# Performance work log

Hardware: AMD Instinct MI355X
Metric: run time of the kernel (lower is better)

Reference implementation:

```python
import jax, jax.numpy as jnp
import numpy as np

N_NODES = 50000
N_EDGES = 400000
N_GRAPHS = 32
EMB = 64
EDGE_DIM = 4
IN_DIM = 11
LAYERS = 4
EPS = 1e-5


def _bn(x, g, b):
    # BatchNorm1d in train mode: biased batch statistics over rows
    m = jnp.mean(x, axis=0)
    v = jnp.mean(jnp.square(x - m), axis=0)
    return g * (x - m) * jax.lax.rsqrt(v + EPS) + b


def setup_inputs() -> dict:
    key = jax.random.key(0)
    ks = jax.random.split(key, 16)
    x = jax.random.normal(ks[0], (N_NODES, IN_DIM), dtype=jnp.float32)
    edge_attr = jax.random.normal(ks[1], (N_EDGES, EDGE_DIM), dtype=jnp.float32)
    edge_index = jax.random.randint(ks[2], (2, N_EDGES), 0, N_NODES, dtype=jnp.int32)
    batch = jnp.sort(jax.random.randint(ks[3], (N_NODES,), 0, N_GRAPHS, dtype=jnp.int32))

    def lin(k, fan_in, shape):
        bound = 1.0 / np.sqrt(fan_in)
        return jax.random.uniform(k, shape, jnp.float32, -bound, bound)

    msg_in = 2 * EMB + EDGE_DIM  # 132
    upd_in = 2 * EMB             # 128
    kk = jax.random.split(ks[4], 12)
    params = dict(
        lin_in_W=lin(kk[0], IN_DIM, (IN_DIM, EMB)),
        lin_in_b=lin(kk[1], IN_DIM, (EMB,)),
        msg_W1=lin(kk[2], msg_in, (LAYERS, msg_in, EMB)),
        msg_b1=lin(kk[3], msg_in, (LAYERS, EMB)),
        msg_g1=jnp.ones((LAYERS, EMB), jnp.float32),
        msg_be1=jnp.zeros((LAYERS, EMB), jnp.float32),
        msg_W2=lin(kk[4], EMB, (LAYERS, EMB, EMB)),
        msg_b2=lin(kk[5], EMB, (LAYERS, EMB)),
        msg_g2=jnp.ones((LAYERS, EMB), jnp.float32),
        msg_be2=jnp.zeros((LAYERS, EMB), jnp.float32),
        upd_W1=lin(kk[6], upd_in, (LAYERS, upd_in, EMB)),
        upd_b1=lin(kk[7], upd_in, (LAYERS, EMB)),
        upd_g1=jnp.ones((LAYERS, EMB), jnp.float32),
        upd_be1=jnp.zeros((LAYERS, EMB), jnp.float32),
        upd_W2=lin(kk[8], EMB, (LAYERS, EMB, EMB)),
        upd_b2=lin(kk[9], EMB, (LAYERS, EMB)),
        upd_g2=jnp.ones((LAYERS, EMB), jnp.float32),
        upd_be2=jnp.zeros((LAYERS, EMB), jnp.float32),
        pred_W=lin(kk[10], EMB, (EMB, 1)),
        pred_b=lin(kk[11], EMB, (1,)),
    )
    return dict(x=x, edge_attr=edge_attr, edge_index=edge_index, batch=batch, **params)


def reference(x, edge_attr, edge_index, batch, lin_in_W, lin_in_b,
              msg_W1, msg_b1, msg_g1, msg_be1, msg_W2, msg_b2, msg_g2, msg_be2,
              upd_W1, upd_b1, upd_g1, upd_be1, upd_W2, upd_b2, upd_g2, upd_be2,
              pred_W, pred_b):
    src = edge_index[0]  # j (source)
    dst = edge_index[1]  # i (target, PyG default flow source_to_target)
    h = x @ lin_in_W + lin_in_b  # (n, d)
    for l in range(LAYERS):
        m_in = jnp.concatenate([h[dst], h[src], edge_attr], axis=-1)  # (e, 2d+d_e)
        m = jax.nn.relu(_bn(m_in @ msg_W1[l] + msg_b1[l], msg_g1[l], msg_be1[l]))
        m = jax.nn.relu(_bn(m @ msg_W2[l] + msg_b2[l], msg_g2[l], msg_be2[l]))
        aggr = jax.ops.segment_sum(m, dst, num_segments=N_NODES)  # scatter-add
        u_in = jnp.concatenate([h, aggr], axis=-1)  # (n, 2d)
        u = jax.nn.relu(_bn(u_in @ upd_W1[l] + upd_b1[l], upd_g1[l], upd_be1[l]))
        u = jax.nn.relu(_bn(u @ upd_W2[l] + upd_b2[l], upd_g2[l], upd_be2[l]))
        h = h + u  # residual in MPNNModel.forward
    sums = jax.ops.segment_sum(h, batch, num_segments=N_GRAPHS)
    counts = jax.ops.segment_sum(jnp.ones((h.shape[0],), h.dtype), batch, num_segments=N_GRAPHS)
    h_graph = sums / jnp.maximum(counts, 1.0)[:, None]  # global_mean_pool
    out = h_graph @ pred_W + pred_b  # (G, 1)
    return out.reshape(-1)
```

## Files before the change

### kernel.cpp

```cpp
#include <hip/hip_runtime.h>

#define DEV __device__ __forceinline__

constexpr int NN = 50000;
constexpr int NE = 400000;
constexpr int NG = 32;
constexpr float EPSV = 1e-5f;
constexpr int SCAN_BLOCKS = 196;
constexpr int NSHARD = 8;
constexpr int STB = NSHARD * 128;

typedef __attribute__((ext_vector_type(8))) short s16x8;
typedef __attribute__((ext_vector_type(4))) float f32x4;

DEV unsigned short f2b(float f) {
  union { float f; unsigned u; } x; x.f = f;
  unsigned r = x.u + 0x7fffu + ((x.u >> 16) & 1u);
  return (unsigned short)(r >> 16);
}
DEV float b2f(unsigned short u) {
  union { unsigned u; float f; } x; x.u = ((unsigned)u) << 16; return x.f;
}

DEV s16x8 frag_from_f32(const float* p) {
  const float4 v0 = *(const float4*)p;
  const float4 v1 = *(const float4*)(p + 4);
  s16x8 af;
  af[0] = (short)f2b(v0.x); af[1] = (short)f2b(v0.y);
  af[2] = (short)f2b(v0.z); af[3] = (short)f2b(v0.w);
  af[4] = (short)f2b(v1.x); af[5] = (short)f2b(v1.y);
  af[6] = (short)f2b(v1.z); af[7] = (short)f2b(v1.w);
  return af;
}

DEV void ld8(float* d, const float* p) {
  float4 a = *(const float4*)p;
  float4 b = *(const float4*)(p + 4);
  d[0] = a.x; d[1] = a.y; d[2] = a.z; d[3] = a.w;
  d[4] = b.x; d[5] = b.y; d[6] = b.z; d[7] = b.w;
}

DEV void bn_coeff(const float* __restrict__ st, const float* __restrict__ g,
                  const float* __restrict__ be, float invM, int c,
                  float& sc, float& sh) {
  float s = 0.f, s2 = 0.f;
#pragma unroll
  for (int k = 0; k < NSHARD; ++k) {
    s += st[k * 128 + c];
    s2 += st[k * 128 + 64 + c];
  }
  float mean = s * invM;
  float var = s2 * invM - mean * mean;
  sc = g[c] * rsqrtf(var + EPSV);
  sh = be[c] - mean * sc;
}

__global__ __launch_bounds__(256) void lin_in_kernel(
    const float* __restrict__ x, const float* __restrict__ W,
    const float* __restrict__ b, float* __restrict__ h)
{
  int gid = blockIdx.x * 256 + threadIdx.x;
  if (gid >= NN * 64) return;
  int n = gid >> 6, c = gid & 63;
  float acc = b[c];
#pragma unroll
  for (int k = 0; k < 11; ++k)
    acc = fmaf(x[n * 11 + k], W[k * 64 + c], acc);
  h[gid] = acc;
}

__global__ __launch_bounds__(256) void hist_kernel(
    const int* __restrict__ dstI, int* __restrict__ deg)
{
  int e = blockIdx.x * 256 + threadIdx.x;
  if (e < NE) atomicAdd(&deg[dstI[e]], 1);
}

__global__ __launch_bounds__(256) void scan_pass1(
    const int* __restrict__ deg, int* __restrict__ blockSums)
{
  __shared__ int red[4];
  int tid = threadIdx.x;
  int idx = blockIdx.x * 256 + tid;
  int v = (idx < NN) ? deg[idx] : 0;
#pragma unroll
  for (int off = 32; off > 0; off >>= 1) v += __shfl_down(v, off, 64);
  if ((tid & 63) == 0) red[tid >> 6] = v;
  __syncthreads();
  if (tid == 0) blockSums[blockIdx.x] = red[0] + red[1] + red[2] + red[3];
}

__global__ __launch_bounds__(256) void scan_pass2(
    const int* __restrict__ blockSums, int* __restrict__ blockOffs)
{
  __shared__ int part[256];
  int tid = threadIdx.x;
  int v = (tid < SCAN_BLOCKS) ? blockSums[tid] : 0;
  part[tid] = v;
  __syncthreads();
  for (int off = 1; off < 256; off <<= 1) {
    int t = 0;
    if (tid >= off) t = part[tid - off];
    __syncthreads();
    if (tid >= off) part[tid] += t;
    __syncthreads();
  }
  blockOffs[tid] = (tid == 0) ? 0 : part[tid - 1];
}

__global__ __launch_bounds__(256) void scan_pass3(
    const int* __restrict__ deg, const int* __restrict__ blockOffs,
    int* __restrict__ rowptr, int* __restrict__ cursor)
{
  __shared__ int part[256];
  int tid = threadIdx.x;
  int idx = blockIdx.x * 256 + tid;
  int v = (idx < NN) ? deg[idx] : 0;
  part[tid] = v;
  __syncthreads();
  for (int off = 1; off < 256; off <<= 1) {
    int t = 0;
    if (tid >= off) t = part[tid - off];
    __syncthreads();
    if (tid >= off) part[tid] += t;
    __syncthreads();
  }
  int excl = (tid == 0) ? 0 : part[tid - 1];
  int val = blockOffs[blockIdx.x] + excl;
  if (idx < NN) { rowptr[idx] = val; cursor[idx] = val; }
  if (idx == 0) rowptr[NN] = NE;
}

__global__ __launch_bounds__(256) void fill_pos_kernel(
    const int* __restrict__ dstI, int* __restrict__ cursor,
    int* __restrict__ eid)
{
  int e = blockIdx.x * 256 + threadIdx.x;
  if (e < NE) {
    int pos = atomicAdd(&cursor[dstI[e]], 1);
    eid[pos] = e;
  }
}

__global__ __launch_bounds__(256) void permute_kernel(
    const int* __restrict__ eid, const int* __restrict__ srcI,
    const int* __restrict__ dstI, const float* __restrict__ ea,
    int* __restrict__ srcP, int* __restrict__ dstP,
    float* __restrict__ eaP)
{
  int p = blockIdx.x * 256 + threadIdx.x;
  if (p < NE) {
    int e = eid[p];
    srcP[p] = srcI[e];
    dstP[p] = dstI[e];
    *(float4*)&eaP[(size_t)p * 4] = *(const float4*)&ea[(size_t)e * 4];
  }
}

__global__ __launch_bounds__(256) void gemm_dual_mfma(
    float* __restrict__ h, const float* __restrict__ W,
    const unsigned short* __restrict__ u2,
    const float* __restrict__ st, const float* __restrict__ g,
    const float* __restrict__ be, float invM,
    unsigned short* __restrict__ Hd, unsigned short* __restrict__ Hs)
{
  __shared__ __align__(16) unsigned short Wt_s[2 * 64 * 72];
  __shared__ float sc_s[64], sh_s[64];

  const int tid = threadIdx.x;
  const int lane = tid & 63;
  const int wave = tid >> 6;
  const int nn = lane & 15;
  const int kq = lane >> 4;

  if (u2 != nullptr && tid < 64) {
    float sc, sh;
    bn_coeff(st, g, be, invM, tid, sc, sh);
    sc_s[tid] = sc;
    sh_s[tid] = sh;
  }
#pragma unroll
  for (int i = 0; i < 32; ++i) {
    int idx = i * 256 + tid;
    int half = idx >> 12;
    int rem = idx & 4095;
    int k = rem >> 6, n = rem & 63;
    Wt_s[half * 4608 + n * 72 + k] = f2b(W[idx]);
  }
  __syncthreads();

  s16x8 bfrag[2][4][2];
#pragma unroll
  for (int o = 0; o < 2; ++o)
#pragma unroll
    for (int nt = 0; nt < 4; ++nt)
#pragma unroll
      for (int kc = 0; kc < 2; ++kc) {
        const unsigned short* p =
            &Wt_s[o * 4608 + (nt * 16 + nn) * 72 + kc * 32 + kq * 8];
#pragma unroll
        for (int j = 0; j < 8; ++j) bfrag[o][nt][kc][j] = (short)p[j];
      }

  const int rbase = blockIdx.x * 128 + wave * 32;

  f32x4 acc[2][2][4];
#pragma unroll
  for (int o = 0; o < 2; ++o)
#pragma unroll
    for (int rt = 0; rt < 2; ++rt)
#pragma unroll
      for (int nt = 0; nt < 4; ++nt) acc[o][rt][nt] = (f32x4){0.f, 0.f, 0.f, 0.f};

#pragma unroll
  for (int rt = 0; rt < 2; ++rt) {
    int row = rbase + rt * 16 + nn;
    int rowc = row < NN ? row : NN - 1;
#pragma unroll
    for (int kc = 0; kc < 2; ++kc) {
      const int c0k = kc * 32 + kq * 8;
      s16x8 af;
      if (u2 != nullptr) {
        float* hp = &h[(size_t)rowc * 64 + c0k];
        float hv[8];
        ld8(hv, hp);
        uint4 uv = *(const uint4*)&u2[(size_t)rowc * 64 + c0k];
        const unsigned uw[4] = {uv.x, uv.y, uv.z, uv.w};
#pragma unroll
        for (int d = 0; d < 4; ++d) {
          union { unsigned u; float f; } lo, hi;
          lo.u = (uw[d] & 0xffffu) << 16;
          hi.u = uw[d] & 0xffff0000u;
          int j0 = d * 2, j1 = d * 2 + 1;
          hv[j0] += fmaxf(fmaf(sc_s[c0k + j0], lo.f, sh_s[c0k + j0]), 0.f);
          hv[j1] += fmaxf(fmaf(sc_s[c0k + j1], hi.f, sh_s[c0k + j1]), 0.f);
        }
        if (row < NN) {
          *(float4*)hp = make_float4(hv[0], hv[1], hv[2], hv[3]);
          *(float4*)(hp + 4) = make_float4(hv[4], hv[5], hv[6], hv[7]);
        }
#pragma unroll
        for (int j = 0; j < 8; ++j) af[j] = (short)f2b(hv[j]);
      } else {
        af = frag_from_f32(&h[(size_t)rowc * 64 + c0k]);
      }
#pragma unroll
      for (int o = 0; o < 2; ++o)
#pragma unroll
        for (int nt = 0; nt < 4; ++nt)
          acc[o][rt][nt] = __builtin_amdgcn_mfma_f32_16x16x32_bf16(
              af, bfrag[o][nt][kc], acc[o][rt][nt], 0, 0, 0);
    }
  }

#pragma unroll
  for (int rt = 0; rt < 2; ++rt)
#pragma unroll
    for (int nt = 0; nt < 4; ++nt) {
      int col = nt * 16 + nn;
#pragma unroll
      for (int reg = 0; reg < 4; ++reg) {
        int row = rbase + rt * 16 + kq * 4 + reg;
        if (row < NN) {
          Hd[(size_t)row * 64 + col] = f2b(acc[0][rt][nt][reg]);
          Hs[(size_t)row * 64 + col] = f2b(acc[1][rt][nt][reg]);
        }
      }
    }
}

__global__ __launch_bounds__(256) void edge_stats(
    const unsigned short* __restrict__ Hd, const unsigned short* __restrict__ Hs,
    const float* __restrict__ eaP, const int* __restrict__ srcP,
    const int* __restrict__ dstP, const float* __restrict__ Wb,
    const float* __restrict__ bias, float* __restrict__ outStats)
{
  __shared__ float red_s[128];
  const int tid = threadIdx.x;
  const int c0 = (tid & 7) * 8;
  float bv[8], w0[8], w1[8], w2[8], w3[8];
#pragma unroll
  for (int j = 0; j < 8; ++j) {
    bv[j] = bias[c0 + j];
    w0[j] = Wb[0 * 64 + c0 + j];
    w1[j] = Wb[1 * 64 + c0 + j];
    w2[j] = Wb[2 * 64 + c0 + j];
    w3[j] = Wb[3 * 64 + c0 + j];
  }

  float s[8], s2[8];
#pragma unroll
  for (int j = 0; j < 8; ++j) { s[j] = 0.f; s2[j] = 0.f; }

  const int e0 = (blockIdx.x * 256 + tid) >> 3;
  const int estep = (gridDim.x * 256) >> 3;

  for (int e = e0; e < NE; e += 4 * estep) {
    bool has[4];
    uint4 hd[4], hs[4];
    float4 av[4];
#pragma unroll
    for (int u = 0; u < 4; ++u) {
      int ee = e + u * estep;
      has[u] = ee < NE;
      int ec = has[u] ? ee : e;
      int si = srcP[ec], di = dstP[ec];
      av[u] = *(const float4*)&eaP[(size_t)ec * 4];
      hd[u] = *(const uint4*)&Hd[(size_t)di * 64 + c0];
      hs[u] = *(const uint4*)&Hs[(size_t)si * 64 + c0];
    }
#pragma unroll
    for (int u = 0; u < 4; ++u) {
      if (!has[u]) continue;
      const unsigned hdw[4] = {hd[u].x, hd[u].y, hd[u].z, hd[u].w};
      const unsigned hsw[4] = {hs[u].x, hs[u].y, hs[u].z, hs[u].w};
#pragma unroll
      for (int d = 0; d < 4; ++d) {
        union { unsigned uu; float f; } a0, a1, b0, b1u;
        a0.uu = (hdw[d] & 0xffffu) << 16; a1.uu = hdw[d] & 0xffff0000u;
        b0.uu = (hsw[d] & 0xffffu) << 16; b1u.uu = hsw[d] & 0xffff0000u;
        int j0 = d * 2, j1 = d * 2 + 1;
        float y0 = a0.f + b0.f + bv[j0] + av[u].x * w0[j0] + av[u].y * w1[j0] + av[u].z * w2[j0] + av[u].w * w3[j0];
        float y1 = a1.f + b1u.f + bv[j1] + av[u].x * w0[j1] + av[u].y * w1[j1] + av[u].z * w2[j1] + av[u].w * w3[j1];
        s[j0] += y0; s2[j0] += y0 * y0;
        s[j1] += y1; s2[j1] += y1 * y1;
      }
    }
  }
#pragma unroll
  for (int j = 0; j < 8; ++j) {
    s[j] += __shfl_xor(s[j], 8, 64);
    s[j] += __shfl_xor(s[j], 16, 64);
    s[j] += __shfl_xor(s[j], 32, 64);
    s2[j] += __shfl_xor(s2[j], 8, 64);
    s2[j] += __shfl_xor(s2[j], 16, 64);
    s2[j] += __shfl_xor(s2[j], 32, 64);
  }
  if (tid < 128) red_s[tid] = 0.f;
  __syncthreads();
  if ((tid & 63) < 8) {
#pragma unroll
    for (int j = 0; j < 8; ++j) {
      atomicAdd(&red_s[c0 + j], s[j]);
      atomicAdd(&red_s[64 + c0 + j], s2[j]);
    }
  }
  __syncthreads();
  if (tid < 128)
    atomicAdd(&outStats[(blockIdx.x & (NSHARD - 1)) * 128 + tid], red_s[tid]);
}

__global__ __launch_bounds__(256) void edge_mlp_fused(
    const unsigned short* __restrict__ Hd, const unsigned short* __restrict__ Hs,
    const float* __restrict__ eaP, const int* __restrict__ srcP,
    const int* __restrict__ dstP,
    const float* __restrict__ Wb,
    const float* __restrict__ b1,
    const float* __restrict__ st0, const float* __restrict__ g1,
    const float* __restrict__ be1, float invE,
    const float* __restrict__ W2,
    const float* __restrict__ b2,
    unsigned short* __restrict__ t2,
    float* __restrict__ outStats)
{
  __shared__ __align__(16) unsigned short Wt_s[64 * 72];
  __shared__ float scs_s[64], bb_s[64], wp_s[4][64];
  __shared__ float red_s[128];

  const int tid = threadIdx.x;
  const int lane = tid & 63;
  const int wave = tid >> 6;
  const int nn = lane & 15;
  const int kq = lane >> 4;

  if (tid < 64) {
    float sc, sh;
    bn_coeff(st0, g1, be1, invE, tid, sc, sh);
    scs_s[tid] = sc;
    bb_s[tid] = fmaf(sc, b1[tid], sh);
    wp_s[0][tid] = sc * Wb[0 * 64 + tid];
    wp_s[1][tid] = sc * Wb[1 * 64 + tid];
    wp_s[2][tid] = sc * Wb[2 * 64 + tid];
    wp_s[3][tid] = sc * Wb[3 * 64 + tid];
  }
#pragma unroll
  for (int i = 0; i < 16; ++i) {
    int idx = i * 256 + tid;
    int k = idx >> 6, n = idx & 63;
    Wt_s[n * 72 + k] = f2b(W2[idx]);
  }
  __syncthreads();

  s16x8 bfrag[4][2];
#pragma unroll
  for (int nt = 0; nt < 4; ++nt)
#pragma unroll
    for (int kc = 0; kc < 2; ++kc)
      bfrag[nt][kc] = *(const s16x8*)&Wt_s[(nt * 16 + nn) * 72 + kc * 32 + kq * 8];

  float bcol[4];
#pragma unroll
  for (int nt = 0; nt < 4; ++nt) bcol[nt] = b2[nt * 16 + nn];

  float s[4] = {0.f, 0.f, 0.f, 0.f};
  float s2[4] = {0.f, 0.f, 0.f, 0.f};

  for (int chunk = 0; chunk < 2; ++chunk) {
    const int rb = blockIdx.x * 512 + chunk * 256 + wave * 64;

    int di4[4], si4[4];
    float4 av4[4];
#pragma unroll
    for (int rt = 0; rt < 4; ++rt) {
      int row = rb + rt * 16 + nn;
      int rowc = row < NE ? row : NE - 1;
      di4[rt] = dstP[rowc];
      si4[rt] = srcP[rowc];
      av4[rt] = *(const float4*)&eaP[(size_t)rowc * 4];
    }

    f32x4 acc[4][4];
#pragma unroll
    for (int rt = 0; rt < 4; ++rt)
#pragma unroll
      for (int nt = 0; nt < 4; ++nt) acc[rt][nt] = (f32x4){0.f, 0.f, 0.f, 0.f};

#pragma unroll
    for (int kc = 0; kc < 2; ++kc) {
      const int c0k = kc * 32 + kq * 8;
      float sc8[8], bb8[8], wv0[8], wv1[8], wv2[8], wv3[8];
      ld8(sc8, &scs_s[c0k]);
      ld8(bb8, &bb_s[c0k]);
      ld8(wv0, &wp_s[0][c0k]);
      ld8(wv1, &wp_s[1][c0k]);
      ld8(wv2, &wp_s[2][c0k]);
      ld8(wv3, &wp_s[3][c0k]);
#pragma unroll
      for (int rt = 0; rt < 4; ++rt) {
        uint4 hd = *(const uint4*)&Hd[(size_t)di4[rt] * 64 + c0k];
        uint4 hs = *(const uint4*)&Hs[(size_t)si4[rt] * 64 + c0k];
        const unsigned hdw[4] = {hd.x, hd.y, hd.z, hd.w};
        const unsigned hsw[4] = {hs.x, hs.y, hs.z, hs.w};
        const float4 av = av4[rt];
        s16x8 af;
#pragma unroll
        for (int d = 0; d < 4; ++d) {
          union { unsigned uu; float f; } a0, a1, b0, b1u;
          a0.uu = (hdw[d] & 0xffffu) << 16; a1.uu = hdw[d] & 0xffff0000u;
          b0.uu = (hsw[d] & 0xffffu) << 16; b1u.uu = hsw[d] & 0xffff0000u;
          int j0 = d * 2, j1 = d * 2 + 1;
          float y0 = fmaf(sc8[j0], a0.f + b0.f, bb8[j0]);
          y0 = fmaf(av.x, wv0[j0], y0); y0 = fmaf(av.y, wv1[j0], y0);
          y0 = fmaf(av.z, wv2[j0], y0); y0 = fmaf(av.w, wv3[j0], y0);
          float y1 = fmaf(sc8[j1], a1.f + b1u.f, bb8[j1]);
          y1 = fmaf(av.x, wv0[j1], y1); y1 = fmaf(av.y, wv1[j1], y1);
          y1 = fmaf(av.z, wv2[j1], y1); y1 = fmaf(av.w, wv3[j1], y1);
          af[j0] = (short)f2b(fmaxf(y0, 0.f));
          af[j1] = (short)f2b(fmaxf(y1, 0.f));
        }
#pragma unroll
        for (int nt = 0; nt < 4; ++nt)
          acc[rt][nt] = __builtin_amdgcn_mfma_f32_16x16x32_bf16(
              af, bfrag[nt][kc], acc[rt][nt], 0, 0, 0);
      }
    }

#pragma unroll
    for (int rt = 0; rt < 4; ++rt)
#pragma unroll
      for (int nt = 0; nt < 4; ++nt) {
        int col = nt * 16 + nn;
#pragma unroll
        for (int reg = 0; reg < 4; ++reg) {
          int row = rb + rt * 16 + kq * 4 + reg;
          if (row < NE) {
            float y = acc[rt][nt][reg] + bcol[nt];
            t2[(size_t)row * 64 + col] = f2b(y);
            s[nt] += y; s2[nt] += y * y;
          }
        }
      }
  }

#pragma unroll
  for (int nt = 0; nt < 4; ++nt) {
    s[nt] += __shfl_xor(s[nt], 16, 64);
    s[nt] += __shfl_xor(s[nt], 32, 64);
    s2[nt] += __shfl_xor(s2[nt], 16, 64);
    s2[nt] += __shfl_xor(s2[nt], 32, 64);
  }
  if (tid < 128) red_s[tid] = 0.f;
  __syncthreads();
  if (lane < 16) {
#pragma unroll
    for (int nt = 0; nt < 4; ++nt) {
      atomicAdd(&red_s[nt * 16 + nn], s[nt]);
      atomicAdd(&red_s[64 + nt * 16 + nn], s2[nt]);
    }
  }
  __syncthreads();
  if (tid < 128)
    atomicAdd(&outStats[(blockIdx.x & (NSHARD - 1)) * 128 + tid], red_s[tid]);
}

__global__ __launch_bounds__(256) void gemm64_bn_mfma(
    const unsigned short* A0,
    const float* __restrict__ W,
    const float* __restrict__ bias,
    const float* __restrict__ inStats,
    const float* __restrict__ inG,
    const float* __restrict__ inBe,
    float invM_in,
    unsigned short* outp,
    float* __restrict__ outStats,
    int M)
{
  __shared__ __align__(16) unsigned short Wt_s[64 * 72];
  __shared__ float scale_s[64];
  __shared__ float shift_s[64];
  __shared__ float red_s[128];

  const int tid = threadIdx.x;
  const int lane = tid & 63;
  const int wave = tid >> 6;
  const int nn = lane & 15;
  const int kq = lane >> 4;

  if (tid < 64) {
    float sc, sh;
    bn_coeff(inStats, inG, inBe, invM_in, tid, sc, sh);
    scale_s[tid] = sc;
    shift_s[tid] = sh;
  }
#pragma unroll
  for (int i = 0; i < 16; ++i) {
    int idx = i * 256 + tid;
    int k = idx >> 6, n = idx & 63;
    Wt_s[n * 72 + k] = f2b(W[idx]);
  }
  __syncthreads();

  s16x8 bfrag[4][2];
#pragma unroll
  for (int nt = 0; nt < 4; ++nt)
#pragma unroll
    for (int kc = 0; kc < 2; ++kc)
      bfrag[nt][kc] = *(const s16x8*)&Wt_s[(nt * 16 + nn) * 72 + kc * 32 + kq * 8];

  float scf[2][8], shf[2][8];
#pragma unroll
  for (int kc = 0; kc < 2; ++kc) {
    int k0 = kc * 32 + kq * 8;
    ld8(scf[kc], &scale_s[k0]);
    ld8(shf[kc], &shift_s[k0]);
  }

  float bcol[4];
#pragma unroll
  for (int nt = 0; nt < 4; ++nt) bcol[nt] = bias[nt * 16 + nn];

  float s[4] = {0.f, 0.f, 0.f, 0.f};
  float s2[4] = {0.f, 0.f, 0.f, 0.f};

  uint4 raw[4][2];
  f32x4 acc[4][4];

  const int rb0 = blockIdx.x * 512 + wave * 64;
#pragma unroll
  for (int rt = 0; rt < 4; ++rt) {
    int row = rb0 + rt * 16 + nn;
    int rowc = row < M ? row : M - 1;
#pragma unroll
    for (int kc = 0; kc < 2; ++kc)
      raw[rt][kc] = *(const uint4*)&A0[(size_t)rowc * 64 + kc * 32 + kq * 8];
  }

#pragma unroll
  for (int rt = 0; rt < 4; ++rt)
#pragma unroll
    for (int nt = 0; nt < 4; ++nt) acc[rt][nt] = (f32x4){0.f, 0.f, 0.f, 0.f};
#pragma unroll
  for (int rt = 0; rt < 4; ++rt) {
#pragma unroll
    for (int kc = 0; kc < 2; ++kc) {
      unsigned wbits[4] = {raw[rt][kc].x, raw[rt][kc].y, raw[rt][kc].z, raw[rt][kc].w};
      s16x8 af;
#pragma unroll
      for (int d = 0; d < 4; ++d) {
        union { unsigned u; float f; } lo, hi;
        lo.u = (wbits[d] & 0xffffu) << 16;
        hi.u = wbits[d] & 0xffff0000u;
        int j0 = d * 2, j1 = d * 2 + 1;
        af[j0] = (short)f2b(fmaxf(fmaf(scf[kc][j0], lo.f, shf[kc][j0]), 0.f));
        af[j1] = (short)f2b(fmaxf(fmaf(scf[kc][j1], hi.f, shf[kc][j1]), 0.f));
      }
#pragma unroll
      for (int nt = 0; nt < 4; ++nt)
        acc[rt][nt] = __builtin_amdgcn_mfma_f32_16x16x32_bf16(
            af, bfrag[nt][kc], acc[rt][nt], 0, 0, 0);
    }
  }

  const int rb1 = rb0 + 256;
#pragma unroll
  for (int rt = 0; rt < 4; ++rt) {
    int row = rb1 + rt * 16 + nn;
    int rowc = row < M ? row : M - 1;
#pragma unroll
    for (int kc = 0; kc < 2; ++kc)
      raw[rt][kc] = *(const uint4*)&A0[(size_t)rowc * 64 + kc * 32 + kq * 8];
  }

#pragma unroll
  for (int rt = 0; rt < 4; ++rt)
#pragma unroll
    for (int nt = 0; nt < 4; ++nt) {
      int col = nt * 16 + nn;
#pragma unroll
      for (int reg = 0; reg < 4; ++reg) {
        int row = rb0 + rt * 16 + kq * 4 + reg;
        if (row < M) {
          float y = acc[rt][nt][reg] + bcol[nt];
          outp[(size_t)row * 64 + col] = f2b(y);
          s[nt] += y; s2[nt] += y * y;
        }
      }
    }

#pragma unroll
  for (int rt = 0; rt < 4; ++rt)
#pragma unroll
    for (int nt = 0; nt < 4; ++nt) acc[rt][nt] = (f32x4){0.f, 0.f, 0.f, 0.f};
#pragma unroll
  for (int rt = 0; rt < 4; ++rt) {
#pragma unroll
    for (int kc = 0; kc < 2; ++kc) {
      unsigned wbits[4] = {raw[rt][kc].x, raw[rt][kc].y, raw[rt][kc].z, raw[rt][kc].w};
      s16x8 af;
#pragma unroll
      for (int d = 0; d < 4; ++d) {
        union { unsigned u; float f; } lo, hi;
        lo.u = (wbits[d] & 0xffffu) << 16;
        hi.u = wbits[d] & 0xffff0000u;
        int j0 = d * 2, j1 = d * 2 + 1;
        af[j0] = (short)f2b(fmaxf(fmaf(scf[kc][j0], lo.f, shf[kc][j0]), 0.f));
        af[j1] = (short)f2b(fmaxf(fmaf(scf[kc][j1], hi.f, shf[kc][j1]), 0.f));
      }
#pragma unroll
      for (int nt = 0; nt < 4; ++nt)
        acc[rt][nt] = __builtin_amdgcn_mfma_f32_16x16x32_bf16(
            af, bfrag[nt][kc], acc[rt][nt], 0, 0, 0);
    }
  }

#pragma unroll
  for (int rt = 0; rt < 4; ++rt)
#pragma unroll
    for (int nt = 0; nt < 4; ++nt) {
      int col = nt * 16 + nn;
#pragma unroll
      for (int reg = 0; reg < 4; ++reg) {
        int row = rb1 + rt * 16 + kq * 4 + reg;
        if (row < M) {
          float y = acc[rt][nt][reg] + bcol[nt];
          outp[(size_t)row * 64 + col] = f2b(y);
          s[nt] += y; s2[nt] += y * y;
        }
      }
    }

#pragma unroll
  for (int nt = 0; nt < 4; ++nt) {
    s[nt] += __shfl_xor(s[nt], 16, 64);
    s[nt] += __shfl_xor(s[nt], 32, 64);
    s2[nt] += __shfl_xor(s2[nt], 16, 64);
    s2[nt] += __shfl_xor(s2[nt], 32, 64);
  }
  if (tid < 128) red_s[tid] = 0.f;
  __syncthreads();
  if (lane < 16) {
#pragma unroll
    for (int nt = 0; nt < 4; ++nt) {
      atomicAdd(&red_s[nt * 16 + nn], s[nt]);
      atomicAdd(&red_s[64 + nt * 16 + nn], s2[nt]);
    }
  }
  __syncthreads();
  if (tid < 128)
    atomicAdd(&outStats[(blockIdx.x & (NSHARD - 1)) * 128 + tid], red_s[tid]);
}

__global__ __launch_bounds__(256) void gemm_concat_mfma(
    const float* __restrict__ A0,
    const unsigned short* __restrict__ A1b,
    const float* __restrict__ W,
    const float* __restrict__ bias,
    unsigned short* __restrict__ outp,
    float* __restrict__ outStats,
    int M)
{
  __shared__ __align__(16) unsigned short Wt_s[64 * 136];
  __shared__ float red_s[128];

  const int tid = threadIdx.x;
  const int lane = tid & 63;
  const int wave = tid >> 6;
  const int nn = lane & 15;
  const int kq = lane >> 4;

#pragma unroll
  for (int i = 0; i < 32; ++i) {
    int idx = i * 256 + tid;
    int k = idx >> 6, n = idx & 63;
    Wt_s[n * 136 + k] = f2b(W[idx]);
  }
  __syncthreads();

  s16x8 bfrag[4][4];
#pragma unroll
  for (int nt = 0; nt < 4; ++nt)
#pragma unroll
    for (int kc = 0; kc < 4; ++kc) {
      const unsigned short* p = &Wt_s[(nt * 16 + nn) * 136 + kc * 32 + kq * 8];
#pragma unroll
      for (int j = 0; j < 8; ++j) bfrag[nt][kc][j] = (short)p[j];
    }

  const int rbase = blockIdx.x * 128 + wave * 32;

  f32x4 acc[2][4];
#pragma unroll
  for (int rt = 0; rt < 2; ++rt)
#pragma unroll
    for (int nt = 0; nt < 4; ++nt) acc[rt][nt] = (f32x4){0.f, 0.f, 0.f, 0.f};

#pragma unroll
  for (int rt = 0; rt < 2; ++rt) {
    int row = rbase + rt * 16 + nn;
    int rowc = row < M ? row : M - 1;
#pragma unroll
    for (int kc = 0; kc < 4; ++kc) {
      s16x8 af;
      if (kc < 2) {
        af = frag_from_f32(&A0[(size_t)rowc * 64 + kc * 32 + kq * 8]);
      } else {
        af = *(const s16x8*)&A1b[(size_t)rowc * 64 + (kc - 2) * 32 + kq * 8];
      }
#pragma unroll
      for (int nt = 0; nt < 4; ++nt)
        acc[rt][nt] = __builtin_amdgcn_mfma_f32_16x16x32_bf16(
            af, bfrag[nt][kc], acc[rt][nt], 0, 0, 0);
    }
  }

  float bcol[4];
#pragma unroll
  for (int nt = 0; nt < 4; ++nt) bcol[nt] = bias[nt * 16 + nn];

  float s[4] = {0.f, 0.f, 0.f, 0.f};
  float s2[4] = {0.f, 0.f, 0.f, 0.f};
#pragma unroll
  for (int rt = 0; rt < 2; ++rt)
#pragma unroll
    for (int nt = 0; nt < 4; ++nt) {
      int col = nt * 16 + nn;
#pragma unroll
      for (int reg = 0; reg < 4; ++reg) {
        int row = rbase + rt * 16 + kq * 4 + reg;
        if (row < M) {
          float y = acc[rt][nt][reg] + bcol[nt];
          outp[(size_t)row * 64 + col] = f2b(y);
          s[nt] += y; s2[nt] += y * y;
        }
      }
    }
#pragma unroll
  for (int nt = 0; nt < 4; ++nt) {
    s[nt] += __shfl_xor(s[nt], 16, 64);
    s[nt] += __shfl_xor(s[nt], 32, 64);
    s2[nt] += __shfl_xor(s2[nt], 16, 64);
    s2[nt] += __shfl_xor(s2[nt], 32, 64);
  }
  if (tid < 128) red_s[tid] = 0.f;
  __syncthreads();
  if (lane < 16) {
#pragma unroll
    for (int nt = 0; nt < 4; ++nt) {
      atomicAdd(&red_s[nt * 16 + nn], s[nt]);
      atomicAdd(&red_s[64 + nt * 16 + nn], s2[nt]);
    }
  }
  __syncthreads();
  if (tid < 128)
    atomicAdd(&outStats[(blockIdx.x & (NSHARD - 1)) * 128 + tid], red_s[tid]);
}

__global__ __launch_bounds__(256) void aggregate_kernel(
    const unsigned short* __restrict__ t2, const int* __restrict__ rowptr,
    const float* __restrict__ stats, const float* __restrict__ g,
    const float* __restrict__ be, float invM,
    unsigned short* __restrict__ aggr)
{
  __shared__ float sc_s[64], sh_s[64];
  const int tid = threadIdx.x;
  if (tid < 64) {
    float sc, sh;
    bn_coeff(stats, g, be, invM, tid, sc, sh);
    sc_s[tid] = sc;
    sh_s[tid] = sh;
  }
  __syncthreads();

  int node = (blockIdx.x * 256 + tid) >> 6;
  int lane = tid & 63;
  if (node >= NN) return;
  const int c8 = (lane & 7) * 8;
  const int rq = lane >> 3;

  float sc[8], sh[8];
#pragma unroll
  for (int j = 0; j < 8; ++j) {
    sc[j] = sc_s[c8 + j];
    sh[j] = sh_s[c8 + j];
  }

  int lo = rowptr[node], hi = rowptr[node + 1];
  float acc[8] = {0.f, 0.f, 0.f, 0.f, 0.f, 0.f, 0.f, 0.f};

  for (int i = lo; i < hi; i += 16) {
    int r0 = i + rq;
    int r1 = i + 8 + rq;
    bool h0 = r0 < hi, h1 = r1 < hi;
    uint4 v0 = make_uint4(0u, 0u, 0u, 0u), v1 = make_uint4(0u, 0u, 0u, 0u);
    if (h0) v0 = *(const uint4*)&t2[(size_t)r0 * 64 + c8];
    if (h1) v1 = *(const uint4*)&t2[(size_t)r1 * 64 + c8];
    if (h0) {
      const unsigned w[4] = {v0.x, v0.y, v0.z, v0.w};
#pragma unroll
      for (int d = 0; d < 4; ++d) {
        union { unsigned u; float f; } a0, a1;
        a0.u = (w[d] & 0xffffu) << 16;
        a1.u = w[d] & 0xffff0000u;
        acc[d * 2] += fmaxf(fmaf(sc[d * 2], a0.f, sh[d * 2]), 0.f);
        acc[d * 2 + 1] += fmaxf(fmaf(sc[d * 2 + 1], a1.f, sh[d * 2 + 1]), 0.f);
      }
    }
    if (h1) {
      const unsigned w[4] = {v1.x, v1.y, v1.z, v1.w};
#pragma unroll
      for (int d = 0; d < 4; ++d) {
        union { unsigned u; float f; } a0, a1;
        a0.u = (w[d] & 0xffffu) << 16;
        a1.u = w[d] & 0xffff0000u;
        acc[d * 2] += fmaxf(fmaf(sc[d * 2], a0.f, sh[d * 2]), 0.f);
        acc[d * 2 + 1] += fmaxf(fmaf(sc[d * 2 + 1], a1.f, sh[d * 2 + 1]), 0.f);
      }
    }
  }
#pragma unroll
  for (int j = 0; j < 8; ++j) {
    acc[j] += __shfl_xor(acc[j], 8, 64);
    acc[j] += __shfl_xor(acc[j], 16, 64);
    acc[j] += __shfl_xor(acc[j], 32, 64);
  }
  if (rq == 0) {
    unsigned short o[8];
#pragma unroll
    for (int j = 0; j < 8; ++j) o[j] = f2b(acc[j]);
    *(uint4*)&aggr[(size_t)node * 64 + c8] = *(const uint4*)o;
  }
}

constexpr int POOL_NPB = 128;

__global__ __launch_bounds__(256) void pool_partial(
    const float* __restrict__ h, const unsigned short* __restrict__ u2,
    const float* __restrict__ st, const float* __restrict__ g,
    const float* __restrict__ be, float invM,
    const int* __restrict__ batch, float* __restrict__ sums)
{
  int lane = threadIdx.x & 63;
  int wave = threadIdx.x >> 6;
  float sc, sh;
  bn_coeff(st, g, be, invM, lane, sc, sh);
  int base = blockIdx.x * POOL_NPB;
  float acc = 0.f;
  int gcur = -1;
  for (int i = wave; i < POOL_NPB; i += 4) {
    int n = base + i;
    if (n >= NN) break;
    int gb = batch[n];
    if (gb != gcur) {
      if (gcur >= 0) atomicAdd(&sums[gcur * 64 + lane], acc);
      gcur = gb;
      acc = 0.f;
    }
    acc += h[(size_t)n * 64 + lane] +
           fmaxf(fmaf(sc, b2f(u2[(size_t)n * 64 + lane]), sh), 0.f);
  }
  if (gcur >= 0) atomicAdd(&sums[gcur * 64 + lane], acc);
}

DEV int lower_bound_i(const int* __restrict__ a, int n, int v) {
  int lo = 0, hi = n;
  while (lo < hi) {
    int m = (lo + hi) >> 1;
    if (a[m] < v) lo = m + 1; else hi = m;
  }
  return lo;
}

__global__ __launch_bounds__(64) void pool_final(
    const float* __restrict__ sums, const int* __restrict__ batch,
    const float* __restrict__ predW, const float* __restrict__ predB,
    float* __restrict__ out)
{
  int g = blockIdx.x;
  int lane = threadIdx.x;
  int lo = lower_bound_i(batch, NN, g);
  int hi = lower_bound_i(batch, NN, g + 1);
  float cnt = fmaxf((float)(hi - lo), 1.0f);
  float p = sums[g * 64 + lane] / cnt * predW[lane];
#pragma unroll
  for (int off = 32; off > 0; off >>= 1) p += __shfl_down(p, off, 64);
  if (lane == 0) out[g] = p + predB[0];
}

extern "C" void kernel_launch(void* const* d_in, const int* in_sizes, int n_in,
                              void* d_out, int out_size, void* d_ws, size_t ws_size,
                              hipStream_t stream)
{
  (void)in_sizes; (void)n_in; (void)out_size; (void)ws_size;

  const float* x        = (const float*)d_in[0];
  const float* edge_attr= (const float*)d_in[1];
  const int*   eidx     = (const int*)d_in[2];
  const int*   batch    = (const int*)d_in[3];
  const float* linW     = (const float*)d_in[4];
  const float* linB     = (const float*)d_in[5];
  const float* msgW1    = (const float*)d_in[6];
  const float* msgB1    = (const float*)d_in[7];
  const float* msgG1    = (const float*)d_in[8];
  const float* msgBe1   = (const float*)d_in[9];
  const float* msgW2    = (const float*)d_in[10];
  const float* msgB2    = (const float*)d_in[11];
  const float* msgG2    = (const float*)d_in[12];
  const float* msgBe2   = (const float*)d_in[13];
  const float* updW1    = (const float*)d_in[14];
  const float* updB1    = (const float*)d_in[15];
  const float* updG1    = (const float*)d_in[16];
  const float* updBe1   = (const float*)d_in[17];
  const float* updW2    = (const float*)d_in[18];
  const float* updB2    = (const float*)d_in[19];
  const float* updG2    = (const float*)d_in[20];
  const float* updBe2   = (const float*)d_in[21];
  const float* predW    = (const float*)d_in[22];
  const float* predB    = (const float*)d_in[23];

  const int* srcI = eidx;
  const int* dstI = eidx + NE;

  char* p = (char*)d_ws;
  float* h  = (float*)p;            p += (size_t)NN * 64 * 4;
  unsigned short* t1 = (unsigned short*)p; p += (size_t)NE * 64 * 2;
  unsigned short* aggr = (unsigned short*)p; p += (size_t)NN * 64 * 2;
  unsigned short* u1 = (unsigned short*)p;   p += (size_t)NN * 64 * 2;
  unsigned short* Hd = (unsigned short*)p;   p += (size_t)NN * 64 * 2;
  unsigned short* Hs = (unsigned short*)p;   p += (size_t)NN * 64 * 2;
  float* stats = (float*)p;         p += 16 * STB * 4;
  float* sums = (float*)p;          p += NG * 64 * 4;
  int* deg = (int*)p;               p += (size_t)NN * 4;
  int* cursor = (int*)p;            p += (size_t)NN * 4;
  int* rowptr = (int*)p;            p += (size_t)(NN + 1) * 4;
  int* eid = (int*)p;               p += (size_t)NE * 4;
  int* srcP = (int*)p;              p += (size_t)NE * 4;
  int* dstP = (int*)p;              p += (size_t)NE * 4;
  float* eaP = (float*)p;           p += (size_t)NE * 4 * 4;
  int* blockSums = (int*)p;         p += 256 * 4;
  int* blockOffs = (int*)p;         p += 256 * 4;

  hipMemsetAsync(stats, 0, (size_t)(16 * STB + NG * 64 + NN) * 4, stream);

  hist_kernel<<<(NE + 255) / 256, 256, 0, stream>>>(dstI, deg);
  scan_pass1<<<SCAN_BLOCKS, 256, 0, stream>>>(deg, blockSums);
  scan_pass2<<<1, 256, 0, stream>>>(blockSums, blockOffs);
  scan_pass3<<<SCAN_BLOCKS, 256, 0, stream>>>(deg, blockOffs, rowptr, cursor);
  fill_pos_kernel<<<(NE + 255) / 256, 256, 0, stream>>>(dstI, cursor, eid);
  permute_kernel<<<(NE + 255) / 256, 256, 0, stream>>>(
      eid, srcI, dstI, edge_attr, srcP, dstP, eaP);

  lin_in_kernel<<<(NN * 64 + 255) / 256, 256, 0, stream>>>(x, linW, linB, h);

  const float invE = 1.0f / (float)NE;
  const float invN = 1.0f / (float)NN;
  const int NB128 = (NN + 127) / 128;
  const int NB512 = (NN + 511) / 512;
  const int EB512 = (NE + 511) / 512;

  for (int l = 0; l < 4; ++l) {
    float* st0 = stats + (l * 4 + 0) * STB;
    float* st1 = stats + (l * 4 + 1) * STB;
    float* st2 = stats + (l * 4 + 2) * STB;
    float* st3 = stats + (l * 4 + 3) * STB;
    const float* W1 = msgW1 + (size_t)l * 132 * 64;

    const unsigned short* prevU2 = (l == 0) ? nullptr : u1;
    const float* pst = (l == 0) ? stats : stats + ((l - 1) * 4 + 3) * STB;
    const float* pg  = (l == 0) ? updG2 : updG2 + (l - 1) * 64;
    const float* pbe = (l == 0) ? updBe2 : updBe2 + (l - 1) * 64;

    gemm_dual_mfma<<<NB128, 256, 0, stream>>>(
        h, W1, prevU2, pst, pg, pbe, invN, Hd, Hs);

    edge_stats<<<2048, 256, 0, stream>>>(
        Hd, Hs, eaP, srcP, dstP, W1 + 128 * 64, msgB1 + l * 64, st0);

    edge_mlp_fused<<<EB512, 256, 0, stream>>>(
        Hd, Hs, eaP, srcP, dstP, W1 + 128 * 64, msgB1 + l * 64,
        st0, msgG1 + l * 64, msgBe1 + l * 64, invE,
        msgW2 + (size_t)l * 64 * 64, msgB2 + l * 64,
        t1, st1);

    aggregate_kernel<<<(NN * 64 + 255) / 256, 256, 0, stream>>>(
        t1, rowptr, st1, msgG2 + l * 64, msgBe2 + l * 64, invE, aggr);

    gemm_concat_mfma<<<NB128, 256, 0, stream>>>(
        h, aggr, updW1 + (size_t)l * 128 * 64, updB1 + l * 64,
        u1, st2, NN);

    gemm64_bn_mfma<<<NB512, 256, 0, stream>>>(
        u1, updW2 + (size_t)l * 64 * 64, updB2 + l * 64,
        st2, updG1 + l * 64, updBe1 + l * 64, invN,
        u1, st3, NN);
  }

  pool_partial<<<(NN + POOL_NPB - 1) / POOL_NPB, 256, 0, stream>>>(
      h, u1, stats + (3 * 4 + 3) * STB, updG2 + 3 * 64, updBe2 + 3 * 64, invN,
      batch, sums);
  pool_final<<<NG, 64, 0, stream>>>(sums, batch, predW, predB, (float*)d_out);
}
```

Baseline: 717.7 us.

## Stage edge activations in LDS with row-coalesced gathers before MFMA

The edge MLP kernel now gathers Hd/Hs rows with eight threads per edge, each reading a contiguous 16-byte slice. It computes the first-layer activation and writes bf16 results into a 256x72 shared-memory tile, then runs the MFMA second layer from LDS. Each block now handles 256 edges instead of 512, so twice as many blocks launch. The intent is more coalesced gathers and more loads in flight, at the cost of about 37KB extra LDS per block, which may lower occupancy, plus an extra barrier.

```diff
diff --git a/kernel.cpp b/kernel.cpp
--- a/kernel.cpp
+++ b/kernel.cpp
@@ -364,6 +364,7 @@
     float* __restrict__ outStats)
 {
   __shared__ __align__(16) unsigned short Wt_s[64 * 72];
+  __shared__ __align__(16) unsigned short af_s[256 * 72];
   __shared__ float scs_s[64], bb_s[64], wp_s[4][64];
   __shared__ float red_s[128];
 
@@ -391,6 +392,64 @@
   }
   __syncthreads();
 
+  const int sl = tid >> 3;
+  const int q  = tid & 7;
+  const int c0 = q * 8;
+  const int rb = blockIdx.x * 256;
+
+  float sc8[8], bb8[8], wv0[8], wv1[8], wv2[8], wv3[8];
+  ld8(sc8, &scs_s[c0]);
+  ld8(bb8, &bb_s[c0]);
+  ld8(wv0, &wp_s[0][c0]);
+  ld8(wv1, &wp_s[1][c0]);
+  ld8(wv2, &wp_s[2][c0]);
+  ld8(wv3, &wp_s[3][c0]);
+
+#pragma unroll
+  for (int ib = 0; ib < 2; ++ib) {
+    int di4[4], si4[4];
+    float4 av4[4];
+    uint4 hd4[4], hs4[4];
+#pragma unroll
+    for (int u = 0; u < 4; ++u) {
+      int r = rb + (ib * 4 + u) * 32 + sl;
+      int rc = r < NE ? r : NE - 1;
+      di4[u] = dstP[rc];
+      si4[u] = srcP[rc];
+      av4[u] = *(const float4*)&eaP[(size_t)rc * 4];
+    }
+#pragma unroll
+    for (int u = 0; u < 4; ++u) {
+      hd4[u] = *(const uint4*)&Hd[(size_t)di4[u] * 64 + c0];
+      hs4[u] = *(const uint4*)&Hs[(size_t)si4[u] * 64 + c0];
+    }
+#pragma unroll
+    for (int u = 0; u < 4; ++u) {
+      const unsigned hdw[4] = {hd4[u].x, hd4[u].y, hd4[u].z, hd4[u].w};
+      const unsigned hsw[4] = {hs4[u].x, hs4[u].y, hs4[u].z, hs4[u].w};
+      const float4 av = av4[u];
+      unsigned short ob[8];
+#pragma unroll
+      for (int d = 0; d < 4; ++d) {
+        union { unsigned uu; float f; } a0, a1, b0, b1u;
+        a0.uu = (hdw[d] & 0xffffu) << 16; a1.uu = hdw[d] & 0xffff0000u;
+        b0.uu = (hsw[d] & 0xffffu) << 16; b1u.uu = hsw[d] & 0xffff0000u;
+        int j0 = d * 2, j1 = d * 2 + 1;
+        float y0 = fmaf(sc8[j0], a0.f + b0.f, bb8[j0]);
+        y0 = fmaf(av.x, wv0[j0], y0); y0 = fmaf(av.y, wv1[j0], y0);
+        y0 = fmaf(av.z, wv2[j0], y0); y0 = fmaf(av.w, wv3[j0], y0);
+        float y1 = fmaf(sc8[j1], a1.f + b1u.f, bb8[j1]);
+        y1 = fmaf(av.x, wv0[j1], y1); y1 = fmaf(av.y, wv1[j1], y1);
+        y1 = fmaf(av.z, wv2[j1], y1); y1 = fmaf(av.w, wv3[j1], y1);
+        ob[j0] = f2b(fmaxf(y0, 0.f));
+        ob[j1] = f2b(fmaxf(y1, 0.f));
+      }
+      *(uint4*)&af_s[(size_t)((ib * 4 + u) * 32 + sl) * 72 + c0] =
+          *(const uint4*)ob;
+    }
+  }
+  __syncthreads();
+
   s16x8 bfrag[4][2];
 #pragma unroll
   for (int nt = 0; nt < 4; ++nt)
@@ -402,85 +461,45 @@
 #pragma unroll
   for (int nt = 0; nt < 4; ++nt) bcol[nt] = b2[nt * 16 + nn];
 
+  const int rw = wave * 64;
+
+  f32x4 acc[4][4];
+#pragma unroll
+  for (int rt = 0; rt < 4; ++rt)
+#pragma unroll
+    for (int nt = 0; nt < 4; ++nt) acc[rt][nt] = (f32x4){0.f, 0.f, 0.f, 0.f};
+
+#pragma unroll
+  for (int rt = 0; rt < 4; ++rt) {
+#pragma unroll
+    for (int kc = 0; kc < 2; ++kc) {
+      s16x8 af = *(const s16x8*)&af_s[(size_t)(rw + rt * 16 + nn) * 72 +
+                                      kc * 32 + kq * 8];
+#pragma unroll
+      for (int nt = 0; nt < 4; ++nt)
+        acc[rt][nt] = __builtin_amdgcn_mfma_f32_16x16x32_bf16(
+            af, bfrag[nt][kc], acc[rt][nt], 0, 0, 0);
+    }
+  }
+
   float s[4] = {0.f, 0.f, 0.f, 0.f};
   float s2[4] = {0.f, 0.f, 0.f, 0.f};
 
-  for (int chunk = 0; chunk < 2; ++chunk) {
-    const int rb = blockIdx.x * 512 + chunk * 256 + wave * 64;
-
-    int di4[4], si4[4];
-    float4 av4[4];
-#pragma unroll
-    for (int rt = 0; rt < 4; ++rt) {
-      int row = rb + rt * 16 + nn;
-      int rowc = row < NE ? row : NE - 1;
-      di4[rt] = dstP[rowc];
-      si4[rt] = srcP[rowc];
-      av4[rt] = *(const float4*)&eaP[(size_t)rowc * 4];
-    }
-
-    f32x4 acc[4][4];
-#pragma unroll
-    for (int rt = 0; rt < 4; ++rt)
-#pragma unroll
-      for (int nt = 0; nt < 4; ++nt) acc[rt][nt] = (f32x4){0.f, 0.f, 0.f, 0.f};
-
-#pragma unroll
-    for (int kc = 0; kc < 2; ++kc) {
-      const int c0k = kc * 32 + kq * 8;
-      float sc8[8], bb8[8], wv0[8], wv1[8], wv2[8], wv3[8];
-      ld8(sc8, &scs_s[c0k]);
-      ld8(bb8, &bb_s[c0k]);
-      ld8(wv0, &wp_s[0][c0k]);
-      ld8(wv1, &wp_s[1][c0k]);
-      ld8(wv2, &wp_s[2][c0k]);
-      ld8(wv3, &wp_s[3][c0k]);
-#pragma unroll
-      for (int rt = 0; rt < 4; ++rt) {
-        uint4 hd = *(const uint4*)&Hd[(size_t)di4[rt] * 64 + c0k];
-        uint4 hs = *(const uint4*)&Hs[(size_t)si4[rt] * 64 + c0k];
-        const unsigned hdw[4] = {hd.x, hd.y, hd.z, hd.w};
-        const unsigned hsw[4] = {hs.x, hs.y, hs.z, hs.w};
-        const float4 av = av4[rt];
-        s16x8 af;
-#pragma unroll
-        for (int d = 0; d < 4; ++d) {
-          union { unsigned uu; float f; } a0, a1, b0, b1u;
-          a0.uu = (hdw[d] & 0xffffu) << 16; a1.uu = hdw[d] & 0xffff0000u;
-          b0.uu = (hsw[d] & 0xffffu) << 16; b1u.uu = hsw[d] & 0xffff0000u;
-          int j0 = d * 2, j1 = d * 2 + 1;
-          float y0 = fmaf(sc8[j0], a0.f + b0.f, bb8[j0]);
-          y0 = fmaf(av.x, wv0[j0], y0); y0 = fmaf(av.y, wv1[j0], y0);
-          y0 = fmaf(av.z, wv2[j0], y0); y0 = fmaf(av.w, wv3[j0], y0);
-          float y1 = fmaf(sc8[j1], a1.f + b1u.f, bb8[j1]);
-          y1 = fmaf(av.x, wv0[j1], y1); y1 = fmaf(av.y, wv1[j1], y1);
-          y1 = fmaf(av.z, wv2[j1], y1); y1 = fmaf(av.w, wv3[j1], y1);
-          af[j0] = (short)f2b(fmaxf(y0, 0.f));
-          af[j1] = (short)f2b(fmaxf(y1, 0.f));
+#pragma unroll
+  for (int rt = 0; rt < 4; ++rt)
+#pragma unroll
+    for (int nt = 0; nt < 4; ++nt) {
+      int col = nt * 16 + nn;
+#pragma unroll
+      for (int reg = 0; reg < 4; ++reg) {
+        int row = rb + rw + rt * 16 + kq * 4 + reg;
+        if (row < NE) {
+          float y = acc[rt][nt][reg] + bcol[nt];
+          t2[(size_t)row * 64 + col] = f2b(y);
+          s[nt] += y; s2[nt] += y * y;
         }
-#pragma unroll
-        for (int nt = 0; nt < 4; ++nt)
-          acc[rt][nt] = __builtin_amdgcn_mfma_f32_16x16x32_bf16(
-              af, bfrag[nt][kc], acc[rt][nt], 0, 0, 0);
-      }
-    }
-
-#pragma unroll
-    for (int rt = 0; rt < 4; ++rt)
-#pragma unroll
-      for (int nt = 0; nt < 4; ++nt) {
-        int col = nt * 16 + nn;
-#pragma unroll
-        for (int reg = 0; reg < 4; ++reg) {
-          int row = rb + rt * 16 + kq * 4 + reg;
-          if (row < NE) {
-            float y = acc[rt][nt][reg] + bcol[nt];
-            t2[(size_t)row * 64 + col] = f2b(y);
-            s[nt] += y; s2[nt] += y * y;
-          }
-        }
-      }
-  }
+      }
+    }
 
 #pragma unroll
   for (int nt = 0; nt < 4; ++nt) {
@@ -995,7 +1014,7 @@
   const float invN = 1.0f / (float)NN;
   const int NB128 = (NN + 127) / 128;
   const int NB512 = (NN + 511) / 512;
-  const int EB512 = (NE + 511) / 512;
+  const int EB256 = (NE + 255) / 256;
 
   for (int l = 0; l < 4; ++l) {
     float* st0 = stats + (l * 4 + 0) * STB;
@@ -1015,7 +1034,7 @@
     edge_stats<<<2048, 256, 0, stream>>>(
         Hd, Hs, eaP, srcP, dstP, W1 + 128 * 64, msgB1 + l * 64, st0);
 
-    edge_mlp_fused<<<EB512, 256, 0, stream>>>(
+    edge_mlp_fused<<<EB256, 256, 0, stream>>>(
         Hd, Hs, eaP, srcP, dstP, W1 + 128 * 64, msgB1 + l * 64,
         st0, msgG1 + l * 64, msgBe1 + l * 64, invE,
         msgW2 + (size_t)l * 64 * 64, msgB2 + l * 64,
```

Result: faster. 676.5 us (-5.7%).
